# Kernel tuning notes

Measured on AMD Instinct MI355X. Metric: run time of the kernel, lower is better.

## Reference

```python
import jax, jax.numpy as jnp
from jax import lax
import numpy as np

B, T, C = 32, 1024, 512
K = 3
MAX_DUR = 4            # durations drawn from [0,5) -> max value 4
L_MAX = T * MAX_DUR    # static padded mel length (torch pads to batch max; we pad to static max)
EPS = 1e-5


def conv_ln_block(x, w, b, g, beta):
    # x: [B,T,C]; torch ConvLNBlock: permute -> Conv1d(SAME) -> relu -> permute -> LayerNorm -> dropout(eval=id)
    y = lax.conv_general_dilated(x.transpose(0, 2, 1), w, (1,), 'SAME',
                                 dimension_numbers=('NCH', 'OIH', 'NCH')) + b[None, :, None]
    y = jax.nn.relu(y).transpose(0, 2, 1)  # [B,T,Cout]
    mu = y.mean(-1, keepdims=True)
    var = y.var(-1, keepdims=True)
    return (y - mu) * lax.rsqrt(var + EPS) * g + beta


def regulate(batch, durations, token_lengths):
    # Vectorized equivalent of DurationRegulator.inflate: repeat token t durations[b,t] times,
    # concatenate, pad. Implemented as cumsum + searchsorted gather (single pass, no ragged loops).
    pos = jnp.arange(T)
    valid = pos[None, :] < token_lengths[:, None]          # [B,T]
    d = jnp.where(valid, durations, 0)
    total = d.sum(axis=1)
    # torch: if durs.sum()==0 -> fill with 1
    d = jnp.where((total == 0)[:, None], valid.astype(d.dtype), d)
    total = d.sum(axis=1)                                   # [B]
    cum = jnp.cumsum(d, axis=1)                             # inclusive cumsum [B,T]
    frames = jnp.arange(L_MAX)
    idx = jax.vmap(lambda c: jnp.searchsorted(c, frames, side='right'))(cum)  # [B,L_MAX]
    idx = jnp.clip(idx, 0, T - 1)
    out = jnp.take_along_axis(batch, idx[:, :, None], axis=1)                 # [B,L_MAX,C]
    frame_mask = frames[None, :] < total[:, None]
    out = out * frame_mask[:, :, None].astype(batch.dtype)
    return out, total.astype(jnp.float32)


def setup_inputs() -> dict:
    key = jax.random.key(0)
    ks = jax.random.split(key, 8)
    batch = jax.random.normal(ks[0], (B, T, C), dtype=jnp.float32)
    token_lengths = jax.random.randint(ks[1], (B,), T // 2, T + 1).astype(jnp.int32)
    mask = jnp.arange(T)[None, :] < token_lengths[:, None]
    label_durations = jax.random.randint(ks[2], (B, T), 0, MAX_DUR + 1).astype(jnp.int32)
    s1 = 1.0 / np.sqrt(C * K)
    s2 = 1.0 / np.sqrt(C * K)
    params = {
        'conv1_w': jax.random.uniform(ks[3], (C, C, K), minval=-s1, maxval=s1, dtype=jnp.float32),
        'conv1_b': jnp.zeros((C,), jnp.float32),
        'ln1_g': jnp.ones((C,), jnp.float32), 'ln1_b': jnp.zeros((C,), jnp.float32),
        'conv2_w': jax.random.uniform(ks[4], (C, C, K), minval=-s2, maxval=s2, dtype=jnp.float32),
        'conv2_b': jnp.zeros((C,), jnp.float32),
        'ln2_g': jnp.ones((C,), jnp.float32), 'ln2_b': jnp.zeros((C,), jnp.float32),
        'lin_w': jax.random.uniform(ks[5], (C, 1), minval=-1/np.sqrt(C), maxval=1/np.sqrt(C), dtype=jnp.float32),
        'lin_b': jnp.zeros((1,), jnp.float32),
    }
    return dict(batch=batch, token_lengths=token_lengths, mask=mask,
                label_durations=label_durations, **params)


def reference(batch, token_lengths, mask, label_durations,
              conv1_w, conv1_b, ln1_g, ln1_b,
              conv2_w, conv2_b, ln2_g, ln2_b,
              lin_w, lin_b):
    # VariancePredictor: two ConvLN blocks + Linear(out_channels, 1), masked fill 0
    h = conv_ln_block(batch, conv1_w, conv1_b, ln1_g, ln1_b)
    h = conv_ln_block(h, conv2_w, conv2_b, ln2_g, ln2_b)
    predicted_durations = h @ lin_w + lin_b                      # [B,T,1]
    predicted_durations = jnp.where(mask[:, :, None], predicted_durations, 0.0)
    # label_durations provided -> regulator uses labels (training path), alpha=1
    padded_batch, mel_lengths = regulate(batch, label_durations, token_lengths)
    return padded_batch, mel_lengths, predicted_durations
```

## Files before the change

### kernel.cpp

```cpp
#include <hip/hip_runtime.h>
#include <hip/hip_bf16.h>
#include <stdint.h>


typedef _Float16 f16;
typedef _Float16 f16x8 __attribute__((ext_vector_type(8)));
typedef float f32x4 __attribute__((ext_vector_type(4)));

#define B_    32
#define T_    1024
#define TP_   1026
#define C_    512
#define LMAX_ 4096
#define KDIM  1536

#define XPAD_OFF   0u
#define H1PAD_OFF  33619968u
#define W1T_OFF    67239936u
#define W2T_OFF    68812800u
#define YWS_OFF    70385664u
#define TOT_OFF    137494528u
#define IDX_OFF    137495040u
#define GWL_OFF    138019328u
#define K12_OFF    138021376u
#define STAT2_OFF  138021888u

#define AS1C(p) ((const __attribute__((address_space(1))) void*)(p))
#define AS3(p)  ((__attribute__((address_space(3))) void*)(p))

#define PP_BLOCKS   2052
#define PW_BLOCKS   256
#define SCAN_BLOCKS 32

__global__ __launch_bounds__(1024) void fused_prep(
        const float* __restrict__ batch, f16* __restrict__ xpad,
        f16* __restrict__ h1pad, const int* __restrict__ tlen,
        const float* __restrict__ w1, const float* __restrict__ w2,
        f16* __restrict__ w1t, f16* __restrict__ w2t,
        const float* __restrict__ g2, const float* __restrict__ be2,
        const float* __restrict__ lw, float* __restrict__ gwl,
        float* __restrict__ k12,
        const int* __restrict__ dur, int* __restrict__ idxarr,
        int* __restrict__ total, float* __restrict__ mel_out) {
    __shared__ int sd[1024];
    __shared__ int sv[1024];
    __shared__ float rk[8][2];
    const int bid = blockIdx.x;
    const int tid = threadIdx.x;

    if (bid < PP_BLOCKS) {
        int row = bid * 16 + (tid >> 6);
        int lane = tid & 63;
        int b = row / TP_, tt = row % TP_;
        size_t dsto = (size_t)row * C_ + lane * 8;
        if (tt == 0 || tt == TP_ - 1) {
            f16x8 z = {};
            *(f16x8*)(xpad + dsto) = z;
            *(f16x8*)(h1pad + dsto) = z;
        } else if (tt <= tlen[b] + 130) {
            const float* src = batch + ((size_t)(b * T_ + tt - 1)) * C_ + lane * 8;
            float4 v0 = ((const float4*)src)[0];
            float4 v1 = ((const float4*)src)[1];
            f16x8 h;
            h[0] = (f16)v0.x; h[1] = (f16)v0.y; h[2] = (f16)v0.z; h[3] = (f16)v0.w;
            h[4] = (f16)v1.x; h[5] = (f16)v1.y; h[6] = (f16)v1.z; h[7] = (f16)v1.w;
            *(f16x8*)(xpad + dsto) = h;
        }
        return;
    }
    if (bid < PP_BLOCKS + PW_BLOCKS) {
        int unit = (bid - PP_BLOCKS) * 4 + (tid >> 8);
        int o = unit & 511;
        const float* w = (unit >> 9) ? w2 : w1;
        f16* wt = (unit >> 9) ? w2t : w1t;
        int tl = tid & 255;
        for (int j = tl; j < KDIM; j += 256) {
            int tap = j >> 9, i = j & 511;
            wt[(size_t)o * KDIM + j] = (f16)w[(size_t)o * KDIM + i * 3 + tap];
        }
        return;
    }
    if (bid < PP_BLOCKS + PW_BLOCKS + SCAN_BLOCKS) {
        int b = bid - (PP_BLOCKS + PW_BLOCKS);
        int t = tid;
        int L = tlen[b];
        int valid = (t < L) ? 1 : 0;
        int d = valid ? dur[b * T_ + t] : 0;
        sd[t] = d; sv[t] = valid;
        __syncthreads();
        for (int off = 1; off < 1024; off <<= 1) {
            int x = 0, y = 0;
            if (t >= off) { x = sd[t - off]; y = sv[t - off]; }
            __syncthreads();
            sd[t] += x; sv[t] += y;
            __syncthreads();
        }
        int totd = sd[1023];
        int cur  = (totd == 0) ? sv[t] : sd[t];
        int prev = (t == 0) ? 0 : ((totd == 0) ? sv[t - 1] : sd[t - 1]);
        for (int f = prev; f < cur; f++) idxarr[b * LMAX_ + f] = t;
        if (t == 1023) {
            int tt = (totd == 0) ? sv[1023] : totd;
            total[b] = tt;
            mel_out[b] = (float)tt;
        }
        return;
    }
    {
        float k1 = 0.f, k2 = 0.f;
        if (tid < C_) {
            float gw_ = g2[tid] * lw[tid];
            gwl[tid] = gw_;
            k1 = gw_;
            k2 = be2[tid] * lw[tid];
        }
#pragma unroll
        for (int m = 32; m; m >>= 1) {
            k1 += __shfl_xor(k1, m, 64);
            k2 += __shfl_xor(k2, m, 64);
        }
        int wv = tid >> 6;
        if ((tid & 63) == 0 && wv < 8) { rk[wv][0] = k1; rk[wv][1] = k2; }
        __syncthreads();
        if (tid == 0) {
            float a1 = 0.f, a2 = 0.f;
#pragma unroll
            for (int i = 0; i < 8; i++) { a1 += rk[i][0]; a2 += rk[i][1]; }
            k12[0] = a1; k12[1] = a2;
        }
    }
}

template<int EPI>
__global__ __launch_bounds__(256, 2) void gemm_k(const f16* __restrict__ A,
                                                 const f16* __restrict__ Bw,
                                                 const float* __restrict__ bias,
                                                 f16* __restrict__ Y,
                                                 const float* __restrict__ gwl,
                                                 float4* __restrict__ stats,
                                                 const int* __restrict__ tlen) {
    __shared__ f16 As[128 * 64];
    __shared__ f16 Bs[256 * 64];
    const int m0 = blockIdx.x * 128;
    {
        const int bb = m0 >> 10, t0 = m0 & 1023;
        const int L = tlen[bb];
        if (EPI == 0 ? (t0 > L) : (t0 >= L)) return;
    }
    const int tid = threadIdx.x;
    const int lane = tid & 63;
    const int w = tid >> 6;
    const int n0 = blockIdx.y * 256;
    const int arow0 = (m0 >> 10) * TP_ + (m0 & 1023);
    const int wm = (w & 1) * 64;
    const int wn = (w >> 1) * 128;

    f32x4 acc[4][8];
#pragma unroll
    for (int i = 0; i < 4; i++)
#pragma unroll
        for (int j = 0; j < 8; j++) acc[i][j] = (f32x4){0.f, 0.f, 0.f, 0.f};

    const int lrow = lane >> 3;
    const int gran = (lane & 7) ^ lrow;
    const f16* aB = A + (size_t)(arow0 + lrow) * C_ + gran * 8;
    const f16* bB = Bw + (size_t)(n0 + lrow) * KDIM + gran * 8;

    for (int kk = 0; kk < KDIM; kk += 64) {
        __syncthreads();
#pragma unroll
        for (int i = 0; i < 4; i++) {
            const int rb = (w + i * 4) * 8;
            __builtin_amdgcn_global_load_lds(AS1C(aB + (size_t)rb * C_ + kk),
                                             AS3(&As[rb * 64]), 16, 0, 0);
        }
#pragma unroll
        for (int j = 0; j < 8; j++) {
            const int rb = (w + j * 4) * 8;
            __builtin_amdgcn_global_load_lds(AS1C(bB + (size_t)rb * KDIM + kk),
                                             AS3(&Bs[rb * 64]), 16, 0, 0);
        }
        __syncthreads();
#pragma unroll
        for (int ks = 0; ks < 2; ks++) {
            const int sl = ((ks << 2) + (lane >> 4)) ^ (lane & 7);
            f16x8 af[4], bf[8];
#pragma unroll
            for (int mi = 0; mi < 4; mi++)
                af[mi] = *(const f16x8*)&As[(wm + mi * 16 + (lane & 15)) * 64 + sl * 8];
#pragma unroll
            for (int ni = 0; ni < 8; ni++)
                bf[ni] = *(const f16x8*)&Bs[(wn + ni * 16 + (lane & 15)) * 64 + sl * 8];
#pragma unroll
            for (int mi = 0; mi < 4; mi++)
#pragma unroll
                for (int ni = 0; ni < 8; ni++)
                    acc[mi][ni] = __builtin_amdgcn_mfma_f32_16x16x32_f16(
                        af[mi], bf[ni], acc[mi][ni], 0, 0, 0);
        }
    }

    const int col = lane & 15;
    const int row4 = (lane >> 4) * 4;

    if (EPI == 0) {
#pragma unroll
        for (int ni = 0; ni < 8; ni++) {
            int n = n0 + wn + ni * 16 + col;
            float bn = bias[n];
#pragma unroll
            for (int mi = 0; mi < 4; mi++) {
#pragma unroll
                for (int r = 0; r < 4; r++) {
                    int m = m0 + wm + mi * 16 + row4 + r;
                    float v = acc[mi][ni][r] + bn;
                    Y[(size_t)m * C_ + n] = (f16)(v > 0.f ? v : 0.f);
                }
            }
        }
    } else {
        float bn[8], gw[8];
#pragma unroll
        for (int ni = 0; ni < 8; ni++) {
            int n = n0 + wn + ni * 16 + col;
            bn[ni] = bias[n];
            gw[ni] = gwl[n];
        }
        float s_[4][4], q_[4][4], u_[4][4];
#pragma unroll
        for (int mi = 0; mi < 4; mi++)
#pragma unroll
            for (int r = 0; r < 4; r++) { s_[mi][r] = 0.f; q_[mi][r] = 0.f; u_[mi][r] = 0.f; }
#pragma unroll
        for (int mi = 0; mi < 4; mi++)
#pragma unroll
            for (int ni = 0; ni < 8; ni++)
#pragma unroll
                for (int r = 0; r < 4; r++) {
                    float v = acc[mi][ni][r] + bn[ni];
                    v = v > 0.f ? v : 0.f;
                    s_[mi][r] += v;
                    q_[mi][r] += v * v;
                    u_[mi][r] += v * gw[ni];
                }
#pragma unroll
        for (int m = 8; m; m >>= 1)
#pragma unroll
            for (int mi = 0; mi < 4; mi++)
#pragma unroll
                for (int r = 0; r < 4; r++) {
                    s_[mi][r] += __shfl_xor(s_[mi][r], m, 64);
                    q_[mi][r] += __shfl_xor(q_[mi][r], m, 64);
                    u_[mi][r] += __shfl_xor(u_[mi][r], m, 64);
                }
        __syncthreads();
        float* red = (float*)As;
        if (col == 0) {
#pragma unroll
            for (int mi = 0; mi < 4; mi++)
#pragma unroll
                for (int r = 0; r < 4; r++) {
                    int row = wm + mi * 16 + row4 + r;
                    int idx = ((w >> 1) * 128 + row) * 3;
                    red[idx]     = s_[mi][r];
                    red[idx + 1] = q_[mi][r];
                    red[idx + 2] = u_[mi][r];
                }
        }
        __syncthreads();
        if (tid < 128) {
            float S = red[tid * 3]     + red[(128 + tid) * 3];
            float Q = red[tid * 3 + 1] + red[(128 + tid) * 3 + 1];
            float U = red[tid * 3 + 2] + red[(128 + tid) * 3 + 2];
            stats[(size_t)(m0 + tid) * 2 + blockIdx.y] = (float4){S, Q, U, 0.f};
        }
    }
}

__global__ __launch_bounds__(256) void ln_kernel(const f16* __restrict__ Y,
                                                 const float* __restrict__ g,
                                                 const float* __restrict__ be,
                                                 f16* __restrict__ hpad,
                                                 const int* __restrict__ tlen) {
    int row = blockIdx.x * 4 + (threadIdx.x >> 6);
    int lane = threadIdx.x & 63;
    int b = row >> 10, t = row & 1023;
    if (t > tlen[b]) return;
    f16x8 yv = *(const f16x8*)(Y + (size_t)row * C_ + lane * 8);
    float v[8];
#pragma unroll
    for (int i = 0; i < 8; i++) v[i] = (float)yv[i];
    float s = 0.f, q = 0.f;
#pragma unroll
    for (int i = 0; i < 8; i++) { s += v[i]; q += v[i] * v[i]; }
#pragma unroll
    for (int m = 32; m; m >>= 1) { s += __shfl_xor(s, m, 64); q += __shfl_xor(q, m, 64); }
    float mu = s * (1.f / 512.f);
    float x = q * (1.f / 512.f) - mu * mu + 1e-5f;
    float rs = rsqrtf(x);
    rs = rs * (1.5f - 0.5f * x * rs * rs);
    const float4 g0 = ((const float4*)g)[lane * 2], g1 = ((const float4*)g)[lane * 2 + 1];
    const float4 e0 = ((const float4*)be)[lane * 2], e1 = ((const float4*)be)[lane * 2 + 1];
    f16x8 h;
    h[0] = (f16)((v[0] - mu) * rs * g0.x + e0.x);
    h[1] = (f16)((v[1] - mu) * rs * g0.y + e0.y);
    h[2] = (f16)((v[2] - mu) * rs * g0.z + e0.z);
    h[3] = (f16)((v[3] - mu) * rs * g0.w + e0.w);
    h[4] = (f16)((v[4] - mu) * rs * g1.x + e1.x);
    h[5] = (f16)((v[5] - mu) * rs * g1.y + e1.y);
    h[6] = (f16)((v[6] - mu) * rs * g1.z + e1.z);
    h[7] = (f16)((v[7] - mu) * rs * g1.w + e1.w);
    *(f16x8*)(hpad + ((size_t)(b * TP_ + t + 1)) * C_ + lane * 8) = h;
}

__global__ __launch_bounds__(256) void gather_fin(const float* __restrict__ batch,
                                                  const int* __restrict__ idxarr,
                                                  const int* __restrict__ total,
                                                  float* __restrict__ out,
                                                  const float4* __restrict__ stats,
                                                  const float* __restrict__ k12,
                                                  const float* __restrict__ lb,
                                                  const int* __restrict__ tlen,
                                                  float* __restrict__ pred) {
    if (blockIdx.x < 32768) {
        int gw = blockIdx.x * 4 + (threadIdx.x >> 6);
        int lane = threadIdx.x & 63;
        int b = gw >> 12;
        int l = gw & (LMAX_ - 1);
        int tot = total[b];
        float4* dst = (float4*)(out + ((size_t)b * LMAX_ + l) * C_);
        if (l < tot) {
            int idx = idxarr[gw];
            const float4* src = (const float4*)(batch + ((size_t)b * T_ + idx) * C_);
            dst[lane] = src[lane];
            dst[lane + 64] = src[lane + 64];
        } else {
            float4 z = {0.f, 0.f, 0.f, 0.f};
            dst[lane] = z;
            dst[lane + 64] = z;
        }
    } else {
        int m = (blockIdx.x - 32768) * 256 + threadIdx.x;
        float4 a = stats[(size_t)m * 2];
        float4 b = stats[(size_t)m * 2 + 1];
        float S = a.x + b.x, Q = a.y + b.y, U = a.z + b.z;
        float mu = S * (1.f / 512.f);
        float x = Q * (1.f / 512.f) - mu * mu + 1e-5f;
        float rs = rsqrtf(x);
        rs = rs * (1.5f - 0.5f * x * rs * rs);
        float p = rs * (U - mu * k12[0]) + k12[1] + lb[0];
        int bb = m >> 10, t = m & 1023;
        pred[m] = (t < tlen[bb]) ? p : 0.f;
    }
}

extern "C" void kernel_launch(void* const* d_in, const int* in_sizes, int n_in,
                              void* d_out, int out_size, void* d_ws, size_t ws_size,
                              hipStream_t stream) {
    const float* batch = (const float*)d_in[0];
    const int* tlen    = (const int*)d_in[1];
    const int* durs    = (const int*)d_in[3];
    const float* w1  = (const float*)d_in[4];
    const float* b1  = (const float*)d_in[5];
    const float* g1  = (const float*)d_in[6];
    const float* be1 = (const float*)d_in[7];
    const float* w2  = (const float*)d_in[8];
    const float* b2  = (const float*)d_in[9];
    const float* g2  = (const float*)d_in[10];
    const float* be2 = (const float*)d_in[11];
    const float* lw  = (const float*)d_in[12];
    const float* lb  = (const float*)d_in[13];

    float* out      = (float*)d_out;
    float* mel_out  = out + (size_t)B_ * LMAX_ * C_;
    float* pred_out = mel_out + B_;

    char* ws    = (char*)d_ws;
    f16* xpad   = (f16*)(ws + XPAD_OFF);
    f16* h1pad  = (f16*)(ws + H1PAD_OFF);
    f16* w1t    = (f16*)(ws + W1T_OFF);
    f16* w2t    = (f16*)(ws + W2T_OFF);
    f16* yws    = (f16*)(ws + YWS_OFF);
    int* tot    = (int*)(ws + TOT_OFF);
    int* idxarr = (int*)(ws + IDX_OFF);
    float* gwl  = (float*)(ws + GWL_OFF);
    float* k12  = (float*)(ws + K12_OFF);
    float4* st2 = (float4*)(ws + STAT2_OFF);

    fused_prep<<<PP_BLOCKS + PW_BLOCKS + SCAN_BLOCKS + 1, 1024, 0, stream>>>(
        batch, xpad, h1pad, tlen, w1, w2, w1t, w2t,
        g2, be2, lw, gwl, k12, durs, idxarr, tot, mel_out);
    gemm_k<0><<<dim3(256, 2), 256, 0, stream>>>(xpad, w1t, b1, yws,
                                                nullptr, nullptr, tlen);
    ln_kernel<<<8192, 256, 0, stream>>>(yws, g1, be1, h1pad, tlen);
    gemm_k<1><<<dim3(256, 2), 256, 0, stream>>>(h1pad, w2t, b2, nullptr,
                                                gwl, st2, tlen);
    gather_fin<<<32768 + 128, 256, 0, stream>>>(batch, idxarr, tot, out,
                                                st2, k12, lb, tlen, pred_out);
}
```

Before: 450.2 us.

## Co-schedule mel gather with first conv GEMM in one launch

Moves the memory-bound regulator gather/zero-fill (32768 blocks) into the same grid as the first conv GEMM, so bandwidth-bound copy blocks and compute-bound MFMA blocks can share the GPU at the same time. The prediction finalization becomes its own small kernel after the second GEMM. The gather blocks now carry the GEMM's large static LDS allocation and launch bounds, which can reduce their occupancy. Gather blocks are placed first in the grid, so the GEMM blocks may only start once most of them have been dispatched.

```diff
diff --git a/kernel.cpp b/kernel.cpp
--- a/kernel.cpp
+++ b/kernel.cpp
@@ -31,6 +31,9 @@
 #define PP_BLOCKS   2052
 #define PW_BLOCKS   256
 #define SCAN_BLOCKS 32
+
+#define GATHER_BLOCKS 32768
+#define G1_BLOCKS     512
 
 __global__ __launch_bounds__(1024) void fused_prep(
         const float* __restrict__ batch, f16* __restrict__ xpad,
@@ -131,21 +134,124 @@
     }
 }
 
-template<int EPI>
-__global__ __launch_bounds__(256, 2) void gemm_k(const f16* __restrict__ A,
-                                                 const f16* __restrict__ Bw,
-                                                 const float* __restrict__ bias,
-                                                 f16* __restrict__ Y,
-                                                 const float* __restrict__ gwl,
-                                                 float4* __restrict__ stats,
-                                                 const int* __restrict__ tlen) {
+__global__ __launch_bounds__(256, 2) void g1_gather(
+        const float* __restrict__ batch, const int* __restrict__ idxarr,
+        const int* __restrict__ total, float* __restrict__ out,
+        const f16* __restrict__ A, const f16* __restrict__ Bw,
+        const float* __restrict__ bias, f16* __restrict__ Y,
+        const int* __restrict__ tlen) {
+    __shared__ f16 As[128 * 64];
+    __shared__ f16 Bs[256 * 64];
+
+    if (blockIdx.x < GATHER_BLOCKS) {
+        int gw = blockIdx.x * 4 + (threadIdx.x >> 6);
+        int lane = threadIdx.x & 63;
+        int b = gw >> 12;
+        int l = gw & (LMAX_ - 1);
+        int tot = total[b];
+        float4* dst = (float4*)(out + ((size_t)b * LMAX_ + l) * C_);
+        if (l < tot) {
+            int idx = idxarr[gw];
+            const float4* src = (const float4*)(batch + ((size_t)b * T_ + idx) * C_);
+            dst[lane] = src[lane];
+            dst[lane + 64] = src[lane + 64];
+        } else {
+            float4 z = {0.f, 0.f, 0.f, 0.f};
+            dst[lane] = z;
+            dst[lane + 64] = z;
+        }
+        return;
+    }
+
+    const int gb = blockIdx.x - GATHER_BLOCKS;
+    const int m0 = (gb & 255) * 128;
+    const int n0 = (gb >> 8) * 256;
+    {
+        const int bb = m0 >> 10, t0 = m0 & 1023;
+        if (t0 > tlen[bb]) return;
+    }
+    const int tid = threadIdx.x;
+    const int lane = tid & 63;
+    const int w = tid >> 6;
+    const int arow0 = (m0 >> 10) * TP_ + (m0 & 1023);
+    const int wm = (w & 1) * 64;
+    const int wn = (w >> 1) * 128;
+
+    f32x4 acc[4][8];
+#pragma unroll
+    for (int i = 0; i < 4; i++)
+#pragma unroll
+        for (int j = 0; j < 8; j++) acc[i][j] = (f32x4){0.f, 0.f, 0.f, 0.f};
+
+    const int lrow = lane >> 3;
+    const int gran = (lane & 7) ^ lrow;
+    const f16* aB = A + (size_t)(arow0 + lrow) * C_ + gran * 8;
+    const f16* bB = Bw + (size_t)(n0 + lrow) * KDIM + gran * 8;
+
+    for (int kk = 0; kk < KDIM; kk += 64) {
+        __syncthreads();
+#pragma unroll
+        for (int i = 0; i < 4; i++) {
+            const int rb = (w + i * 4) * 8;
+            __builtin_amdgcn_global_load_lds(AS1C(aB + (size_t)rb * C_ + kk),
+                                             AS3(&As[rb * 64]), 16, 0, 0);
+        }
+#pragma unroll
+        for (int j = 0; j < 8; j++) {
+            const int rb = (w + j * 4) * 8;
+            __builtin_amdgcn_global_load_lds(AS1C(bB + (size_t)rb * KDIM + kk),
+                                             AS3(&Bs[rb * 64]), 16, 0, 0);
+        }
+        __syncthreads();
+#pragma unroll
+        for (int ks = 0; ks < 2; ks++) {
+            const int sl = ((ks << 2) + (lane >> 4)) ^ (lane & 7);
+            f16x8 af[4], bf[8];
+#pragma unroll
+            for (int mi = 0; mi < 4; mi++)
+                af[mi] = *(const f16x8*)&As[(wm + mi * 16 + (lane & 15)) * 64 + sl * 8];
+#pragma unroll
+            for (int ni = 0; ni < 8; ni++)
+                bf[ni] = *(const f16x8*)&Bs[(wn + ni * 16 + (lane & 15)) * 64 + sl * 8];
+#pragma unroll
+            for (int mi = 0; mi < 4; mi++)
+#pragma unroll
+                for (int ni = 0; ni < 8; ni++)
+                    acc[mi][ni] = __builtin_amdgcn_mfma_f32_16x16x32_f16(
+                        af[mi], bf[ni], acc[mi][ni], 0, 0, 0);
+        }
+    }
+
+    const int col = lane & 15;
+    const int row4 = (lane >> 4) * 4;
+#pragma unroll
+    for (int ni = 0; ni < 8; ni++) {
+        int n = n0 + wn + ni * 16 + col;
+        float bn = bias[n];
+#pragma unroll
+        for (int mi = 0; mi < 4; mi++) {
+#pragma unroll
+            for (int r = 0; r < 4; r++) {
+                int m = m0 + wm + mi * 16 + row4 + r;
+                float v = acc[mi][ni][r] + bn;
+                Y[(size_t)m * C_ + n] = (f16)(v > 0.f ? v : 0.f);
+            }
+        }
+    }
+}
+
+__global__ __launch_bounds__(256, 2) void gemm2_k(const f16* __restrict__ A,
+                                                  const f16* __restrict__ Bw,
+                                                  const float* __restrict__ bias,
+                                                  const float* __restrict__ gwl,
+                                                  float4* __restrict__ stats,
+                                                  const int* __restrict__ tlen) {
     __shared__ f16 As[128 * 64];
     __shared__ f16 Bs[256 * 64];
     const int m0 = blockIdx.x * 128;
     {
         const int bb = m0 >> 10, t0 = m0 & 1023;
-        const int L = tlen[bb];
-        if (EPI == 0 ? (t0 > L) : (t0 >= L)) return;
+        if (t0 >= tlen[bb]) return;
     }
     const int tid = threadIdx.x;
     const int lane = tid & 63;
@@ -203,77 +309,60 @@
     const int col = lane & 15;
     const int row4 = (lane >> 4) * 4;
 
-    if (EPI == 0) {
-#pragma unroll
-        for (int ni = 0; ni < 8; ni++) {
-            int n = n0 + wn + ni * 16 + col;
-            float bn = bias[n];
-#pragma unroll
-            for (int mi = 0; mi < 4; mi++) {
-#pragma unroll
-                for (int r = 0; r < 4; r++) {
-                    int m = m0 + wm + mi * 16 + row4 + r;
-                    float v = acc[mi][ni][r] + bn;
-                    Y[(size_t)m * C_ + n] = (f16)(v > 0.f ? v : 0.f);
-                }
+    float bn[8], gw[8];
+#pragma unroll
+    for (int ni = 0; ni < 8; ni++) {
+        int n = n0 + wn + ni * 16 + col;
+        bn[ni] = bias[n];
+        gw[ni] = gwl[n];
+    }
+    float s_[4][4], q_[4][4], u_[4][4];
+#pragma unroll
+    for (int mi = 0; mi < 4; mi++)
+#pragma unroll
+        for (int r = 0; r < 4; r++) { s_[mi][r] = 0.f; q_[mi][r] = 0.f; u_[mi][r] = 0.f; }
+#pragma unroll
+    for (int mi = 0; mi < 4; mi++)
+#pragma unroll
+        for (int ni = 0; ni < 8; ni++)
+#pragma unroll
+            for (int r = 0; r < 4; r++) {
+                float v = acc[mi][ni][r] + bn[ni];
+                v = v > 0.f ? v : 0.f;
+                s_[mi][r] += v;
+                q_[mi][r] += v * v;
+                u_[mi][r] += v * gw[ni];
             }
-        }
-    } else {
-        float bn[8], gw[8];
-#pragma unroll
-        for (int ni = 0; ni < 8; ni++) {
-            int n = n0 + wn + ni * 16 + col;
-            bn[ni] = bias[n];
-            gw[ni] = gwl[n];
-        }
-        float s_[4][4], q_[4][4], u_[4][4];
+#pragma unroll
+    for (int m = 8; m; m >>= 1)
 #pragma unroll
         for (int mi = 0; mi < 4; mi++)
 #pragma unroll
-            for (int r = 0; r < 4; r++) { s_[mi][r] = 0.f; q_[mi][r] = 0.f; u_[mi][r] = 0.f; }
+            for (int r = 0; r < 4; r++) {
+                s_[mi][r] += __shfl_xor(s_[mi][r], m, 64);
+                q_[mi][r] += __shfl_xor(q_[mi][r], m, 64);
+                u_[mi][r] += __shfl_xor(u_[mi][r], m, 64);
+            }
+    __syncthreads();
+    float* red = (float*)As;
+    if (col == 0) {
 #pragma unroll
         for (int mi = 0; mi < 4; mi++)
 #pragma unroll
-            for (int ni = 0; ni < 8; ni++)
-#pragma unroll
-                for (int r = 0; r < 4; r++) {
-                    float v = acc[mi][ni][r] + bn[ni];
-                    v = v > 0.f ? v : 0.f;
-                    s_[mi][r] += v;
-                    q_[mi][r] += v * v;
-                    u_[mi][r] += v * gw[ni];
-                }
-#pragma unroll
-        for (int m = 8; m; m >>= 1)
-#pragma unroll
-            for (int mi = 0; mi < 4; mi++)
-#pragma unroll
-                for (int r = 0; r < 4; r++) {
-                    s_[mi][r] += __shfl_xor(s_[mi][r], m, 64);
-                    q_[mi][r] += __shfl_xor(q_[mi][r], m, 64);
-                    u_[mi][r] += __shfl_xor(u_[mi][r], m, 64);
-                }
-        __syncthreads();
-        float* red = (float*)As;
-        if (col == 0) {
-#pragma unroll
-            for (int mi = 0; mi < 4; mi++)
-#pragma unroll
-                for (int r = 0; r < 4; r++) {
-                    int row = wm + mi * 16 + row4 + r;
-                    int idx = ((w >> 1) * 128 + row) * 3;
-                    red[idx]     = s_[mi][r];
-                    red[idx + 1] = q_[mi][r];
-                    red[idx + 2] = u_[mi][r];
-                }
-        }
-        __syncthreads();
-        if (tid < 128) {
-            float S = red[tid * 3]     + red[(128 + tid) * 3];
-            float Q = red[tid * 3 + 1] + red[(128 + tid) * 3 + 1];
-            float U = red[tid * 3 + 2] + red[(128 + tid) * 3 + 2];
-            stats[(size_t)(m0 + tid) * 2 + blockIdx.y] = (float4){S, Q, U, 0.f};
-        }
+            for (int r = 0; r < 4; r++) {
+                int row = wm + mi * 16 + row4 + r;
+                int idx = ((w >> 1) * 128 + row) * 3;
+                red[idx]     = s_[mi][r];
+                red[idx + 1] = q_[mi][r];
+                red[idx + 2] = u_[mi][r];
+            }
+    }
+    __syncthreads();
+    if (tid < 128) {
+        float S = red[tid * 3]     + red[(128 + tid) * 3];
+        float Q = red[tid * 3 + 1] + red[(128 + tid) * 3 + 1];
+        float U = red[tid * 3 + 2] + red[(128 + tid) * 3 + 2];
+        stats[(size_t)(m0 + tid) * 2 + blockIdx.y] = (float4){S, Q, U, 0.f};
     }
 }
 
@@ -313,45 +402,22 @@
     *(f16x8*)(hpad + ((size_t)(b * TP_ + t + 1)) * C_ + lane * 8) = h;
 }
 
-__global__ __launch_bounds__(256) void gather_fin(const float* __restrict__ batch,
-                                                  const int* __restrict__ idxarr,
-                                                  const int* __restrict__ total,
-                                                  float* __restrict__ out,
-                                                  const float4* __restrict__ stats,
-                                                  const float* __restrict__ k12,
-                                                  const float* __restrict__ lb,
-                                                  const int* __restrict__ tlen,
-                                                  float* __restrict__ pred) {
-    if (blockIdx.x < 32768) {
-        int gw = blockIdx.x * 4 + (threadIdx.x >> 6);
-        int lane = threadIdx.x & 63;
-        int b = gw >> 12;
-        int l = gw & (LMAX_ - 1);
-        int tot = total[b];
-        float4* dst = (float4*)(out + ((size_t)b * LMAX_ + l) * C_);
-        if (l < tot) {
-            int idx = idxarr[gw];
-            const float4* src = (const float4*)(batch + ((size_t)b * T_ + idx) * C_);
-            dst[lane] = src[lane];
-            dst[lane + 64] = src[lane + 64];
-        } else {
-            float4 z = {0.f, 0.f, 0.f, 0.f};
-            dst[lane] = z;
-            dst[lane + 64] = z;
-        }
-    } else {
-        int m = (blockIdx.x - 32768) * 256 + threadIdx.x;
-        float4 a = stats[(size_t)m * 2];
-        float4 b = stats[(size_t)m * 2 + 1];
-        float S = a.x + b.x, Q = a.y + b.y, U = a.z + b.z;
-        float mu = S * (1.f / 512.f);
-        float x = Q * (1.f / 512.f) - mu * mu + 1e-5f;
-        float rs = rsqrtf(x);
-        rs = rs * (1.5f - 0.5f * x * rs * rs);
-        float p = rs * (U - mu * k12[0]) + k12[1] + lb[0];
-        int bb = m >> 10, t = m & 1023;
-        pred[m] = (t < tlen[bb]) ? p : 0.f;
-    }
+__global__ __launch_bounds__(256) void finalize2(const float4* __restrict__ stats,
+                                                 const float* __restrict__ k12,
+                                                 const float* __restrict__ lb,
+                                                 const int* __restrict__ tlen,
+                                                 float* __restrict__ pred) {
+    int m = blockIdx.x * 256 + threadIdx.x;
+    float4 a = stats[(size_t)m * 2];
+    float4 b = stats[(size_t)m * 2 + 1];
+    float S = a.x + b.x, Q = a.y + b.y, U = a.z + b.z;
+    float mu = S * (1.f / 512.f);
+    float x = Q * (1.f / 512.f) - mu * mu + 1e-5f;
+    float rs = rsqrtf(x);
+    rs = rs * (1.5f - 0.5f * x * rs * rs);
+    float p = rs * (U - mu * k12[0]) + k12[1] + lb[0];
+    int bb = m >> 10, t = m & 1023;
+    pred[m] = (t < tlen[bb]) ? p : 0.f;
 }
 
 extern "C" void kernel_launch(void* const* d_in, const int* in_sizes, int n_in,
@@ -390,11 +456,9 @@
     fused_prep<<<PP_BLOCKS + PW_BLOCKS + SCAN_BLOCKS + 1, 1024, 0, stream>>>(
         batch, xpad, h1pad, tlen, w1, w2, w1t, w2t,
         g2, be2, lw, gwl, k12, durs, idxarr, tot, mel_out);
-    gemm_k<0><<<dim3(256, 2), 256, 0, stream>>>(xpad, w1t, b1, yws,
-                                                nullptr, nullptr, tlen);
+    g1_gather<<<GATHER_BLOCKS + G1_BLOCKS, 256, 0, stream>>>(
+        batch, idxarr, tot, out, xpad, w1t, b1, yws, tlen);
     ln_kernel<<<8192, 256, 0, stream>>>(yws, g1, be1, h1pad, tlen);
-    gemm_k<1><<<dim3(256, 2), 256, 0, stream>>>(h1pad, w2t, b2, nullptr,
-                                                gwl, st2, tlen);
-    gather_fin<<<32768 + 128, 256, 0, stream>>>(batch, idxarr, tot, out,
-                                                st2, k12, lb, tlen, pred_out);
-}
+    gemm2_k<<<dim3(256, 2), 256, 0, stream>>>(h1pad, w2t, b2, gwl, st2, tlen);
+    finalize2<<<128, 256, 0, stream>>>(st2, k12, lb, tlen, pred_out);
+}
```

Result: slower. 477.0 us (+5.9%).

## Pre-swizzle weights into MFMA fragment order and load B directly to registers

Applied to the files above, without the earlier changes.

The weight transpose kernel now writes conv weights in per-lane MFMA fragment order. The GEMM then reads the B operand straight from global memory into registers with coalesced 16-byte loads, so the B shared-memory tile and its LDS reads go away. The warp tiling also changes from 2x2 (64x128 per warp) to 1x4, where each warp covers all 128 rows and 64 columns. This frees LDS and cuts LDS traffic, but B loads are no longer staged and may add global latency that is not overlapped, and the reduction in the LayerNorm-statistics epilogue now sums over four warps.

```diff
diff --git a/kernel.cpp b/kernel.cpp
--- a/kernel.cpp
+++ b/kernel.cpp
@@ -13,6 +13,7 @@
 #define C_    512
 #define LMAX_ 4096
 #define KDIM  1536
+#define NKT   24
 
 #define XPAD_OFF   0u
 #define H1PAD_OFF  33619968u
@@ -31,6 +32,7 @@
 #define PP_BLOCKS   2052
 #define PW_BLOCKS   256
 #define SCAN_BLOCKS 32
+#define FRAGS_PER_M 98304
 
 __global__ __launch_bounds__(1024) void fused_prep(
         const float* __restrict__ batch, f16* __restrict__ xpad,
@@ -69,14 +71,26 @@
         return;
     }
     if (bid < PP_BLOCKS + PW_BLOCKS) {
-        int unit = (bid - PP_BLOCKS) * 4 + (tid >> 8);
-        int o = unit & 511;
-        const float* w = (unit >> 9) ? w2 : w1;
-        f16* wt = (unit >> 9) ? w2t : w1t;
-        int tl = tid & 255;
-        for (int j = tl; j < KDIM; j += 256) {
-            int tap = j >> 9, i = j & 511;
-            wt[(size_t)o * KDIM + j] = (f16)w[(size_t)o * KDIM + i * 3 + tap];
+        int gid = (bid - PP_BLOCKS) * 1024 + tid;
+        if (gid < 2 * FRAGS_PER_M) {
+            const float* w = (gid >= FRAGS_PER_M) ? w2 : w1;
+            f16* wt = (gid >= FRAGS_PER_M) ? w2t : w1t;
+            int fid = (gid >= FRAGS_PER_M) ? gid - FRAGS_PER_M : gid;
+            int kt   = fid >> 12;
+            int rem  = fid & 4095;
+            int nt   = rem >> 7;
+            int rem2 = rem & 127;
+            int ks   = rem2 >> 6;
+            int l    = rem2 & 63;
+            int o     = nt * 16 + (l & 15);
+            int kbase = kt * 64 + (((ks << 2) + (l >> 4)) << 3);
+            int tap   = kbase >> 9;
+            int i0    = kbase & 511;
+            const float* src = w + (size_t)o * KDIM + (size_t)i0 * 3 + tap;
+            f16x8 h;
+#pragma unroll
+            for (int j = 0; j < 8; j++) h[j] = (f16)src[j * 3];
+            *(f16x8*)(wt + (size_t)fid * 8) = h;
         }
         return;
     }
@@ -133,14 +147,13 @@
 
 template<int EPI>
 __global__ __launch_bounds__(256, 2) void gemm_k(const f16* __restrict__ A,
-                                                 const f16* __restrict__ Bw,
+                                                 const f16* __restrict__ B2,
                                                  const float* __restrict__ bias,
                                                  f16* __restrict__ Y,
                                                  const float* __restrict__ gwl,
                                                  float4* __restrict__ stats,
                                                  const int* __restrict__ tlen) {
     __shared__ f16 As[128 * 64];
-    __shared__ f16 Bs[256 * 64];
     const int m0 = blockIdx.x * 128;
     {
         const int bb = m0 >> 10, t0 = m0 & 1023;
@@ -152,21 +165,20 @@
     const int w = tid >> 6;
     const int n0 = blockIdx.y * 256;
     const int arow0 = (m0 >> 10) * TP_ + (m0 & 1023);
-    const int wm = (w & 1) * 64;
-    const int wn = (w >> 1) * 128;
-
-    f32x4 acc[4][8];
-#pragma unroll
-    for (int i = 0; i < 4; i++)
-#pragma unroll
-        for (int j = 0; j < 8; j++) acc[i][j] = (f32x4){0.f, 0.f, 0.f, 0.f};
+    const int nt0 = (n0 >> 4) + w * 4;
+
+    f32x4 acc[8][4];
+#pragma unroll
+    for (int i = 0; i < 8; i++)
+#pragma unroll
+        for (int j = 0; j < 4; j++) acc[i][j] = (f32x4){0.f, 0.f, 0.f, 0.f};
 
     const int lrow = lane >> 3;
     const int gran = (lane & 7) ^ lrow;
     const f16* aB = A + (size_t)(arow0 + lrow) * C_ + gran * 8;
-    const f16* bB = Bw + (size_t)(n0 + lrow) * KDIM + gran * 8;
-
-    for (int kk = 0; kk < KDIM; kk += 64) {
+
+    for (int kt = 0; kt < NKT; ++kt) {
+        const int kk = kt * 64;
         __syncthreads();
 #pragma unroll
         for (int i = 0; i < 4; i++) {
@@ -174,29 +186,28 @@
             __builtin_amdgcn_global_load_lds(AS1C(aB + (size_t)rb * C_ + kk),
                                              AS3(&As[rb * 64]), 16, 0, 0);
         }
-#pragma unroll
-        for (int j = 0; j < 8; j++) {
-            const int rb = (w + j * 4) * 8;
-            __builtin_amdgcn_global_load_lds(AS1C(bB + (size_t)rb * KDIM + kk),
-                                             AS3(&Bs[rb * 64]), 16, 0, 0);
-        }
-        __syncthreads();
+        __syncthreads();
+
+        f16x8 bf0[4], bf1[4];
+#pragma unroll
+        for (int ni = 0; ni < 4; ni++) {
+            const size_t base = ((size_t)((kt * 32 + nt0 + ni) * 2) << 9) + lane * 8;
+            bf0[ni] = *(const f16x8*)&B2[base];
+            bf1[ni] = *(const f16x8*)&B2[base + 512];
+        }
 #pragma unroll
         for (int ks = 0; ks < 2; ks++) {
             const int sl = ((ks << 2) + (lane >> 4)) ^ (lane & 7);
-            f16x8 af[4], bf[8];
-#pragma unroll
-            for (int mi = 0; mi < 4; mi++)
-                af[mi] = *(const f16x8*)&As[(wm + mi * 16 + (lane & 15)) * 64 + sl * 8];
-#pragma unroll
-            for (int ni = 0; ni < 8; ni++)
-                bf[ni] = *(const f16x8*)&Bs[(wn + ni * 16 + (lane & 15)) * 64 + sl * 8];
-#pragma unroll
-            for (int mi = 0; mi < 4; mi++)
-#pragma unroll
-                for (int ni = 0; ni < 8; ni++)
+            f16x8 af[8];
+#pragma unroll
+            for (int mi = 0; mi < 8; mi++)
+                af[mi] = *(const f16x8*)&As[(mi * 16 + (lane & 15)) * 64 + sl * 8];
+#pragma unroll
+            for (int mi = 0; mi < 8; mi++)
+#pragma unroll
+                for (int ni = 0; ni < 4; ni++)
                     acc[mi][ni] = __builtin_amdgcn_mfma_f32_16x16x32_f16(
-                        af[mi], bf[ni], acc[mi][ni], 0, 0, 0);
+                        af[mi], ks ? bf1[ni] : bf0[ni], acc[mi][ni], 0, 0, 0);
         }
     }
 
@@ -205,36 +216,36 @@
 
     if (EPI == 0) {
 #pragma unroll
-        for (int ni = 0; ni < 8; ni++) {
-            int n = n0 + wn + ni * 16 + col;
+        for (int ni = 0; ni < 4; ni++) {
+            int n = n0 + w * 64 + ni * 16 + col;
             float bn = bias[n];
 #pragma unroll
-            for (int mi = 0; mi < 4; mi++) {
+            for (int mi = 0; mi < 8; mi++) {
 #pragma unroll
                 for (int r = 0; r < 4; r++) {
-                    int m = m0 + wm + mi * 16 + row4 + r;
+                    int m = m0 + mi * 16 + row4 + r;
                     float v = acc[mi][ni][r] + bn;
                     Y[(size_t)m * C_ + n] = (f16)(v > 0.f ? v : 0.f);
                 }
             }
         }
     } else {
-        float bn[8], gw[8];
-#pragma unroll
-        for (int ni = 0; ni < 8; ni++) {
-            int n = n0 + wn + ni * 16 + col;
+        float bn[4], gw[4];
+#pragma unroll
+        for (int ni = 0; ni < 4; ni++) {
+            int n = n0 + w * 64 + ni * 16 + col;
             bn[ni] = bias[n];
             gw[ni] = gwl[n];
         }
-        float s_[4][4], q_[4][4], u_[4][4];
-#pragma unroll
-        for (int mi = 0; mi < 4; mi++)
+        float s_[8][4], q_[8][4], u_[8][4];
+#pragma unroll
+        for (int mi = 0; mi < 8; mi++)
 #pragma unroll
             for (int r = 0; r < 4; r++) { s_[mi][r] = 0.f; q_[mi][r] = 0.f; u_[mi][r] = 0.f; }
 #pragma unroll
-        for (int mi = 0; mi < 4; mi++)
-#pragma unroll
-            for (int ni = 0; ni < 8; ni++)
+        for (int mi = 0; mi < 8; mi++)
+#pragma unroll
+            for (int ni = 0; ni < 4; ni++)
 #pragma unroll
                 for (int r = 0; r < 4; r++) {
                     float v = acc[mi][ni][r] + bn[ni];
@@ -246,7 +257,7 @@
 #pragma unroll
         for (int m = 8; m; m >>= 1)
 #pragma unroll
-            for (int mi = 0; mi < 4; mi++)
+            for (int mi = 0; mi < 8; mi++)
 #pragma unroll
                 for (int r = 0; r < 4; r++) {
                     s_[mi][r] += __shfl_xor(s_[mi][r], m, 64);
@@ -257,11 +268,11 @@
         float* red = (float*)As;
         if (col == 0) {
 #pragma unroll
-            for (int mi = 0; mi < 4; mi++)
+            for (int mi = 0; mi < 8; mi++)
 #pragma unroll
                 for (int r = 0; r < 4; r++) {
-                    int row = wm + mi * 16 + row4 + r;
-                    int idx = ((w >> 1) * 128 + row) * 3;
+                    int row = mi * 16 + row4 + r;
+                    int idx = (w * 128 + row) * 3;
                     red[idx]     = s_[mi][r];
                     red[idx + 1] = q_[mi][r];
                     red[idx + 2] = u_[mi][r];
@@ -269,9 +280,12 @@
         }
         __syncthreads();
         if (tid < 128) {
-            float S = red[tid * 3]     + red[(128 + tid) * 3];
-            float Q = red[tid * 3 + 1] + red[(128 + tid) * 3 + 1];
-            float U = red[tid * 3 + 2] + red[(128 + tid) * 3 + 2];
+            float S = 0.f, Q = 0.f, U = 0.f;
+#pragma unroll
+            for (int wv = 0; wv < 4; wv++) {
+                int idx = (wv * 128 + tid) * 3;
+                S += red[idx]; Q += red[idx + 1]; U += red[idx + 2];
+            }
             stats[(size_t)(m0 + tid) * 2 + blockIdx.y] = (float4){S, Q, U, 0.f};
         }
     }
```

After: 467.3 us. +3.8%, slower.

## Triple-buffer GEMM K-loop with async LDS loads and remap workgroups across XCDs

Applied to the files above, without the earlier changes.

The conv GEMM now uses a three-stage LDS ring with K-step 32 instead of a single buffer with K-step 64. The next-next tile is prefetched via global_load_lds while the current tile is computed, using explicit vmcnt waits and raw barriers. The grid is flattened to 1D and block ids are remapped so neighbouring tiles are spread round-robin over the 8 XCDs to improve L2 reuse. This adds LDS usage (72KB per block), which may lower occupancy below the declared two blocks per CU. The hand-counted vmcnt values must match the exact load count per stage.

```diff
diff --git a/kernel.cpp b/kernel.cpp
--- a/kernel.cpp
+++ b/kernel.cpp
@@ -13,6 +13,7 @@
 #define C_    512
 #define LMAX_ 4096
 #define KDIM  1536
+#define NK    48
 
 #define XPAD_OFF   0u
 #define H1PAD_OFF  33619968u
@@ -139,9 +140,18 @@
                                                  const float* __restrict__ gwl,
                                                  float4* __restrict__ stats,
                                                  const int* __restrict__ tlen) {
-    __shared__ f16 As[128 * 64];
-    __shared__ f16 Bs[256 * 64];
-    const int m0 = blockIdx.x * 128;
+    __shared__ f16 lds_[36864];
+    f16* const A0 = lds_;
+    f16* const A1 = lds_ + 4096;
+    f16* const A2 = lds_ + 8192;
+    f16* const B0 = lds_ + 12288;
+    f16* const B1 = lds_ + 20480;
+    f16* const B2 = lds_ + 28672;
+
+    const int bid = blockIdx.x;
+    const int wg  = (bid & 7) * 64 + (bid >> 3);
+    const int m0  = (wg >> 1) * 128;
+    const int n0  = (wg & 1) * 256;
     {
         const int bb = m0 >> 10, t0 = m0 & 1023;
         const int L = tlen[bb];
@@ -150,10 +160,9 @@
     const int tid = threadIdx.x;
     const int lane = tid & 63;
     const int w = tid >> 6;
-    const int n0 = blockIdx.y * 256;
-    const int arow0 = (m0 >> 10) * TP_ + (m0 & 1023);
     const int wm = (w & 1) * 64;
     const int wn = (w >> 1) * 128;
+    const int arow0 = (m0 >> 10) * TP_ + (m0 & 1023);
 
     f32x4 acc[4][8];
 #pragma unroll
@@ -161,44 +170,69 @@
 #pragma unroll
         for (int j = 0; j < 8; j++) acc[i][j] = (f32x4){0.f, 0.f, 0.f, 0.f};
 
-    const int lrow = lane >> 3;
-    const int gran = (lane & 7) ^ lrow;
-    const f16* aB = A + (size_t)(arow0 + lrow) * C_ + gran * 8;
-    const f16* bB = Bw + (size_t)(n0 + lrow) * KDIM + gran * 8;
-
-    for (int kk = 0; kk < KDIM; kk += 64) {
-        __syncthreads();
-#pragma unroll
-        for (int i = 0; i < 4; i++) {
-            const int rb = (w + i * 4) * 8;
-            __builtin_amdgcn_global_load_lds(AS1C(aB + (size_t)rb * C_ + kk),
-                                             AS3(&As[rb * 64]), 16, 0, 0);
-        }
-#pragma unroll
-        for (int j = 0; j < 8; j++) {
-            const int rb = (w + j * 4) * 8;
-            __builtin_amdgcn_global_load_lds(AS1C(bB + (size_t)rb * KDIM + kk),
-                                             AS3(&Bs[rb * 64]), 16, 0, 0);
-        }
-        __syncthreads();
-#pragma unroll
-        for (int ks = 0; ks < 2; ks++) {
-            const int sl = ((ks << 2) + (lane >> 4)) ^ (lane & 7);
-            f16x8 af[4], bf[8];
-#pragma unroll
-            for (int mi = 0; mi < 4; mi++)
-                af[mi] = *(const f16x8*)&As[(wm + mi * 16 + (lane & 15)) * 64 + sl * 8];
-#pragma unroll
-            for (int ni = 0; ni < 8; ni++)
-                bf[ni] = *(const f16x8*)&Bs[(wn + ni * 16 + (lane & 15)) * 64 + sl * 8];
-#pragma unroll
-            for (int mi = 0; mi < 4; mi++)
-#pragma unroll
-                for (int ni = 0; ni < 8; ni++)
-                    acc[mi][ni] = __builtin_amdgcn_mfma_f32_16x16x32_f16(
-                        af[mi], bf[ni], acc[mi][ni], 0, 0, 0);
-        }
-    }
+    const int perm = (lane & 3) ^ ((lane >> 2) & 3) ^ ((lane >> 4) & 3);
+    const int rdo = perm * 8;
+    const f16* aB = A + (size_t)(arow0 + (lane >> 2)) * C_ + perm * 8;
+    const f16* bB = Bw + (size_t)(n0 + (lane >> 2)) * KDIM + perm * 8;
+
+#define STAGE(Ad, Bd, kofs) do {                                              \
+        _Pragma("unroll")                                                     \
+        for (int i_ = 0; i_ < 2; i_++) {                                      \
+            const int rb = (w + i_ * 4) * 16;                                 \
+            __builtin_amdgcn_global_load_lds(                                 \
+                AS1C(aB + (size_t)rb * C_ + (kofs)),                          \
+                AS3((Ad) + rb * 32), 16, 0, 0);                               \
+        }                                                                     \
+        _Pragma("unroll")                                                     \
+        for (int j_ = 0; j_ < 4; j_++) {                                      \
+            const int rb = (w + j_ * 4) * 16;                                 \
+            __builtin_amdgcn_global_load_lds(                                 \
+                AS1C(bB + (size_t)rb * KDIM + (kofs)),                        \
+                AS3((Bd) + rb * 32), 16, 0, 0);                               \
+        }                                                                     \
+    } while (0)
+
+#define COMPUTE(Ac, Bc) do {                                                  \
+        f16x8 af[4], bf[8];                                                   \
+        _Pragma("unroll")                                                     \
+        for (int mi = 0; mi < 4; mi++)                                        \
+            af[mi] = *(const f16x8*)&(Ac)[(wm + mi * 16 + (lane & 15)) * 32 + rdo]; \
+        _Pragma("unroll")                                                     \
+        for (int ni = 0; ni < 8; ni++)                                        \
+            bf[ni] = *(const f16x8*)&(Bc)[(wn + ni * 16 + (lane & 15)) * 32 + rdo]; \
+        _Pragma("unroll")                                                     \
+        for (int mi = 0; mi < 4; mi++)                                        \
+            _Pragma("unroll")                                                 \
+            for (int ni = 0; ni < 8; ni++)                                    \
+                acc[mi][ni] = __builtin_amdgcn_mfma_f32_16x16x32_f16(         \
+                    af[mi], bf[ni], acc[mi][ni], 0, 0, 0);                    \
+    } while (0)
+
+#define ITER(Ac, Bc, tval, DO_STAGE, An2, Bn2, VMSTR) do {                    \
+        if (DO_STAGE) STAGE(An2, Bn2, ((tval) + 2) * 32);                     \
+        asm volatile("s_waitcnt " VMSTR ::: "memory");                        \
+        __builtin_amdgcn_s_barrier();                                         \
+        __builtin_amdgcn_sched_barrier(0);                                    \
+        COMPUTE(Ac, Bc);                                                      \
+        __builtin_amdgcn_sched_barrier(0);                                    \
+        __builtin_amdgcn_s_barrier();                                         \
+    } while (0)
+
+    STAGE(A0, B0, 0);
+    STAGE(A1, B1, 32);
+
+    for (int tt = 0; tt < NK - 3; tt += 3) {
+        ITER(A0, B0, tt,     1, A2, B2, "vmcnt(12)");
+        ITER(A1, B1, tt + 1, 1, A0, B0, "vmcnt(12)");
+        ITER(A2, B2, tt + 2, 1, A1, B1, "vmcnt(12)");
+    }
+    ITER(A0, B0, NK - 3, 1, A2, B2, "vmcnt(12)");
+    ITER(A1, B1, NK - 2, 0, A0, B0, "vmcnt(6)");
+    ITER(A2, B2, NK - 1, 0, A1, B1, "vmcnt(0)");
+
+#undef ITER
+#undef COMPUTE
+#undef STAGE
 
     const int col = lane & 15;
     const int row4 = (lane >> 4) * 4;
@@ -254,7 +288,7 @@
                     u_[mi][r] += __shfl_xor(u_[mi][r], m, 64);
                 }
         __syncthreads();
-        float* red = (float*)As;
+        float* red = (float*)A0;
         if (col == 0) {
 #pragma unroll
             for (int mi = 0; mi < 4; mi++)
@@ -272,7 +306,7 @@
             float S = red[tid * 3]     + red[(128 + tid) * 3];
             float Q = red[tid * 3 + 1] + red[(128 + tid) * 3 + 1];
             float U = red[tid * 3 + 2] + red[(128 + tid) * 3 + 2];
-            stats[(size_t)(m0 + tid) * 2 + blockIdx.y] = (float4){S, Q, U, 0.f};
+            stats[(size_t)(m0 + tid) * 2 + (wg & 1)] = (float4){S, Q, U, 0.f};
         }
     }
 }
@@ -390,11 +424,11 @@
     fused_prep<<<PP_BLOCKS + PW_BLOCKS + SCAN_BLOCKS + 1, 1024, 0, stream>>>(
         batch, xpad, h1pad, tlen, w1, w2, w1t, w2t,
         g2, be2, lw, gwl, k12, durs, idxarr, tot, mel_out);
-    gemm_k<0><<<dim3(256, 2), 256, 0, stream>>>(xpad, w1t, b1, yws,
-                                                nullptr, nullptr, tlen);
+    gemm_k<0><<<512, 256, 0, stream>>>(xpad, w1t, b1, yws,
+                                       nullptr, nullptr, tlen);
     ln_kernel<<<8192, 256, 0, stream>>>(yws, g1, be1, h1pad, tlen);
-    gemm_k<1><<<dim3(256, 2), 256, 0, stream>>>(h1pad, w2t, b2, nullptr,
-                                                gwl, st2, tlen);
+    gemm_k<1><<<512, 256, 0, stream>>>(h1pad, w2t, b2, nullptr,
+                                       gwl, st2, tlen);
     gather_fin<<<32768 + 128, 256, 0, stream>>>(batch, idxarr, tot, out,
                                                 st2, k12, lb, tlen, pred_out);
 }
```

After: 456.9 us. No clear change (+1.5%).
